# Kernel optimization log

Hardware: AMD Instinct MI355X
Metric: run time of the kernel (lower is better)

Reference implementation:

```python
import jax, jax.numpy as jnp
import numpy as np

EMBED_DIM = 400
HEAD_SIZE = 64


def setup_inputs() -> dict:
    key = jax.random.key(0)
    k1, k2, k3, k4 = jax.random.split(key, 4)
    B, T, C = 8, 2048, EMBED_DIM
    x = jax.random.normal(k1, (B, T, C), dtype=jnp.float32)
    # Linear(embed_dim, head_size, bias=False) weights, stored as [C, H] for x @ W
    s = 1.0 / np.sqrt(C)
    Wq = jax.random.uniform(k2, (C, HEAD_SIZE), dtype=jnp.float32, minval=-s, maxval=s)
    Wk = jax.random.uniform(k3, (C, HEAD_SIZE), dtype=jnp.float32, minval=-s, maxval=s)
    Wv = jax.random.uniform(k4, (C, HEAD_SIZE), dtype=jnp.float32, minval=-s, maxval=s)
    return {"x": x, "Wq": Wq, "Wk": Wk, "Wv": Wv}


def reference(x, Wq, Wk, Wv):
    B, T, C = x.shape
    q = x @ Wq  # [B,T,H]
    k = x @ Wk  # [B,T,H]
    v = x @ Wv  # [B,T,H]
    scale = 1.0 / jnp.sqrt(jnp.asarray(q.shape[-1], q.dtype))
    scores = jnp.einsum('bth,bsh->bts', q, k) * scale  # [B,T,T]
    causal = jnp.tril(jnp.ones((T, T), dtype=bool))
    scores = jnp.where(causal, scores, jnp.asarray(-jnp.inf, scores.dtype))
    attn = jax.nn.softmax(scores, axis=-1)
    out = jnp.einsum('bts,bsh->bth', attn, v)  # [B,T,H]
    return out
```

## Files before the change

kernel.cpp:

```cpp
#include <hip/hip_runtime.h>
#include <math.h>

#define B_SZ   8
#define T_SEQ  2048
#define C_DIM  400
#define H_DIM  64
#define NROWS  (B_SZ * T_SEQ)
#define QT_TILES (T_SEQ / 64)
#define KPAD   416
#define LDSTR  424
#define NCH    8
#define TPC    4

typedef short s8v  __attribute__((ext_vector_type(8)));
typedef float f32x4 __attribute__((ext_vector_type(4)));

__device__ __forceinline__ unsigned short f2bf(float f) {
    unsigned int u = __float_as_uint(f);
    u = (u + 0x7FFFu + ((u >> 16) & 1u)) >> 16;
    return (unsigned short)u;
}

__device__ __forceinline__ unsigned cvtpk_bf16(float lo, float hi) {
    unsigned r;
    asm("v_cvt_pk_bf16_f32 %0, %1, %2" : "=v"(r) : "v"(lo), "v"(hi));
    return r;
}

__global__ __launch_bounds__(256) void wprep_kernel(
    const float* __restrict__ Wq, const float* __restrict__ Wk,
    const float* __restrict__ Wv, unsigned short* __restrict__ Wt)
{
    int idx = blockIdx.x * 256 + threadIdx.x;
    if (idx >= 3 * H_DIM * KPAD) return;
    int m = idx / (H_DIM * KPAD);
    int r = idx - m * (H_DIM * KPAD);
    int h = r / KPAD;
    int k = r - h * KPAD;
    const float* W = (m == 0) ? Wq : (m == 1) ? Wk : Wv;
    float v = (k < C_DIM) ? W[k * H_DIM + h] : 0.0f;
    if (m == 0) v *= 0.125f * 1.44269504088896f;
    Wt[idx] = f2bf(v);
}

__global__ __launch_bounds__(256) void proj_kernel(
    const float* __restrict__ x, const unsigned short* __restrict__ Wt,
    unsigned short* __restrict__ Qb, unsigned short* __restrict__ Kb,
    unsigned short* __restrict__ Vt)
{
    __shared__ unsigned short xl[16 * LDSTR];
    const int tid = threadIdx.x;
    const int tile = blockIdx.x;

    const float4* __restrict__ x4 = (const float4*)x;
    for (int idx = tid; idx < 16 * 104; idx += 256) {
        int row = idx / 104, c4 = idx - row * 104;
        ushort4 w;
        if (c4 < 100) {
            float4 v = x4[(size_t)(tile * 16 + row) * 100 + c4];
            w.x = f2bf(v.x); w.y = f2bf(v.y); w.z = f2bf(v.z); w.w = f2bf(v.w);
        } else { w.x = w.y = w.z = w.w = 0; }
        *(ushort4*)&xl[row * LDSTR + c4 * 4] = w;
    }
    __syncthreads();

    const int w = tid >> 6, l = tid & 63;
    const int lr = l & 15, g = l >> 4;

    f32x4 acc[3];
    acc[0] = (f32x4)0.f; acc[1] = (f32x4)0.f; acc[2] = (f32x4)0.f;

    for (int ks = 0; ks < KPAD / 32; ++ks) {
        s8v a = *(const s8v*)&xl[lr * LDSTR + ks * 32 + g * 8];
#pragma unroll
        for (int fl = 0; fl < 3; ++fl) {
            int f = w * 3 + fl;
            int col = (f & 3) * 16 + lr;
            const s8v b = *(const s8v*)&Wt[((size_t)(f >> 2) * H_DIM + col) * KPAD
                                           + ks * 32 + g * 8];
            acc[fl] = __builtin_amdgcn_mfma_f32_16x16x32_bf16(a, b, acc[fl], 0, 0, 0);
        }
    }

#pragma unroll
    for (int fl = 0; fl < 3; ++fl) {
        int f = w * 3 + fl;
        int m = f >> 2, col = (f & 3) * 16 + lr;
#pragma unroll
        for (int r = 0; r < 4; ++r) {
            int row_g = tile * 16 + g * 4 + r;
            unsigned short bv = f2bf(acc[fl][r]);
            if (m == 0)      Qb[(size_t)row_g * H_DIM + col] = bv;
            else if (m == 1) Kb[(size_t)row_g * H_DIM + col] = bv;
            else {
                int b = row_g >> 11, t = row_g & 2047;
                Vt[((size_t)b * H_DIM + col) * T_SEQ + t] = bv;
            }
        }
    }
}

__global__ __launch_bounds__(256) void attn_kernel(
    const unsigned short* __restrict__ Qb, const unsigned short* __restrict__ Kb,
    const unsigned short* __restrict__ Vt,
    float* __restrict__ Opart, float* __restrict__ lpart)
{
    const int c  = blockIdx.x;
    const int qt = blockIdx.y;
    const int b  = blockIdx.z;
    if (c * TPC > qt) return;
    const int kt0 = c * TPC;
    const int kend = min(kt0 + (TPC - 1), qt);

    __shared__ char smem[2][16384];

    const int tid = threadIdx.x;
    const int w = tid >> 6, l = tid & 63;
    const int lr = l & 15, g = l >> 4;
    const int q0 = qt * 64 + w * 16;

    const int r0 = tid >> 3;
    const int ch = tid & 7;
    const int swz = (ch * 16) ^ ((r0 & 7) << 4);
    const char* const Kg = (const char*)(Kb + (size_t)b * T_SEQ * H_DIM);
    const char* const Vg = (const char*)(Vt + (size_t)b * H_DIM * T_SEQ);

    uint4 kA, kB, vA, vB;
    auto LD = [&](int kt) {
        kA = *(const uint4*)(Kg + (size_t)(kt * 64 + r0     ) * 128 + ch * 16);
        kB = *(const uint4*)(Kg + (size_t)(kt * 64 + r0 + 32) * 128 + ch * 16);
        vA = *(const uint4*)(Vg + (size_t)(r0     ) * 4096 + kt * 128 + ch * 16);
        vB = *(const uint4*)(Vg + (size_t)(r0 + 32) * 4096 + kt * 128 + ch * 16);
    };
    auto ST = [&](int buf) {
        char* Kl = smem[buf];
        char* Vl = smem[buf] + 8192;
        *(uint4*)(Kl + r0 * 128 + swz)        = kA;
        *(uint4*)(Kl + (r0 + 32) * 128 + swz) = kB;
        *(uint4*)(Vl + r0 * 128 + swz)        = vA;
        *(uint4*)(Vl + (r0 + 32) * 128 + swz) = vB;
    };

    s8v aq[2];
#pragma unroll
    for (int s = 0; s < 2; ++s)
        aq[s] = *(const s8v*)&Qb[((size_t)b * T_SEQ + q0 + lr) * H_DIM + s * 32 + g * 8];

    f32x4 acc[4];
#pragma unroll
    for (int f = 0; f < 4; ++f) acc[f] = (f32x4)0.f;
    float lsum = 0.f;

    LD(kt0); ST(0);
    __syncthreads();
    int cur = 0;

    for (int kt = kt0; kt <= kend; ++kt) {
        if (kt < kend) LD(kt + 1);
        char* const Kl = smem[cur];
        char* const Vl = smem[cur] + 8192;

        f32x4 sacc[4];
#pragma unroll
        for (int f = 0; f < 4; ++f) sacc[f] = (f32x4)0.f;
        __builtin_amdgcn_s_setprio(1);
#pragma unroll
        for (int f = 0; f < 4; ++f)
#pragma unroll
            for (int s = 0; s < 2; ++s) {
                const s8v ak = *(const s8v*)(Kl + (f * 16 + lr) * 128
                                             + (((s * 4 + g) * 16) ^ ((lr & 7) << 4)));
                sacc[f] = __builtin_amdgcn_mfma_f32_16x16x32_bf16(ak, aq[s], sacc[f], 0, 0, 0);
            }
        __builtin_amdgcn_s_setprio(0);

        float p[4][4];
        const bool diag = (kt == qt);
        const int q_my = q0 + lr;
#pragma unroll
        for (int f = 0; f < 4; ++f)
#pragma unroll
            for (int r = 0; r < 4; ++r) {
                float pv = __builtin_amdgcn_exp2f(sacc[f][r]);
                if (diag && (kt * 64 + f * 16 + g * 4 + r) > q_my) pv = 0.0f;
                p[f][r] = pv;
                lsum += pv;
            }

        s8v ap[2];
#pragma unroll
        for (int s = 0; s < 2; ++s) {
            unsigned Fa = cvtpk_bf16(p[2 * s][0],     p[2 * s][1]);
            unsigned Fb = cvtpk_bf16(p[2 * s][2],     p[2 * s][3]);
            unsigned Ga = cvtpk_bf16(p[2 * s + 1][0], p[2 * s + 1][1]);
            unsigned Gb = cvtpk_bf16(p[2 * s + 1][2], p[2 * s + 1][3]);
            asm("v_permlane32_swap_b32 %0, %1" : "+v"(Fa), "+v"(Ga));
            asm("v_permlane16_swap_b32 %0, %1" : "+v"(Fa), "+v"(Ga));
            asm("v_permlane32_swap_b32 %0, %1" : "+v"(Fb), "+v"(Gb));
            asm("v_permlane16_swap_b32 %0, %1" : "+v"(Fb), "+v"(Gb));
            unsigned wds[4] = { Fa, Fb, Ga, Gb };
            ap[s] = *(const s8v*)wds;
        }

        __builtin_amdgcn_s_setprio(1);
#pragma unroll
        for (int f = 0; f < 4; ++f)
#pragma unroll
            for (int s = 0; s < 2; ++s) {
                const s8v bv = *(const s8v*)(Vl + (f * 16 + lr) * 128
                                             + (((s * 4 + g) * 16) ^ ((lr & 7) << 4)));
                acc[f] = __builtin_amdgcn_mfma_f32_16x16x32_bf16(ap[s], bv, acc[f], 0, 0, 0);
            }
        __builtin_amdgcn_s_setprio(0);

        if (kt < kend) {
            ST(cur ^ 1);
            __syncthreads();
            cur ^= 1;
        }
    }

    lsum += __shfl_xor(lsum, 16, 64);
    lsum += __shfl_xor(lsum, 32, 64);

    const size_t pb = ((size_t)(b * QT_TILES + qt) * NCH + c);
#pragma unroll
    for (int f = 0; f < 4; ++f)
#pragma unroll
        for (int r = 0; r < 4; ++r)
            Opart[pb * 4096 + (w * 16 + g * 4 + r) * 64 + f * 16 + lr] = acc[f][r];
    if (l < 16)
        lpart[pb * 64 + w * 16 + l] = lsum;
}

__global__ __launch_bounds__(256) void combine_kernel(
    const float* __restrict__ Opart, const float* __restrict__ lpart,
    float* __restrict__ out)
{
    const int idx = blockIdx.x * 256 + threadIdx.x;
    const int row = idx >> 4, h4 = idx & 15;
    const int b = row >> 11, t = row & 2047;
    const int qt = t >> 6, r = t & 63;
    const int nch = (qt >> 2) + 1;

    const float4* __restrict__ Op4 = (const float4*)Opart;
    float4 os = make_float4(0.f, 0.f, 0.f, 0.f);
    float ls = 0.f;
    const size_t base = (size_t)(b * QT_TILES + qt) * NCH;
    for (int cc = 0; cc < nch; ++cc) {
        float4 v = Op4[(base + cc) * 1024 + r * 16 + h4];
        os.x += v.x; os.y += v.y; os.z += v.z; os.w += v.w;
        ls += lpart[(base + cc) * 64 + r];
    }
    float inv = 1.0f / ls;
    ((float4*)out)[idx] = make_float4(os.x * inv, os.y * inv, os.z * inv, os.w * inv);
}

extern "C" void kernel_launch(void* const* d_in, const int* in_sizes, int n_in,
                              void* d_out, int out_size, void* d_ws, size_t ws_size,
                              hipStream_t stream)
{
    const float* x  = (const float*)d_in[0];
    const float* Wq = (const float*)d_in[1];
    const float* Wk = (const float*)d_in[2];
    const float* Wv = (const float*)d_in[3];
    float* out = (float*)d_out;

    char* ws = (char*)d_ws;
    unsigned short* Wt = (unsigned short*)(ws);
    unsigned short* Qb = (unsigned short*)(ws + 163840);
    unsigned short* Kb = (unsigned short*)(ws + 163840 + 2097152);
    unsigned short* Vt = (unsigned short*)(ws + 163840 + 2 * 2097152);
    float* Opart = (float*)(ws + 163840 + 3 * 2097152);
    float* lpart = (float*)(ws + 163840 + 3 * 2097152 + 33554432);

    wprep_kernel<<<(3 * H_DIM * KPAD + 255) / 256, 256, 0, stream>>>(Wq, Wk, Wv, Wt);
    proj_kernel<<<NROWS / 16, 256, 0, stream>>>(x, Wt, Qb, Kb, Vt);
    attn_kernel<<<dim3(NCH, QT_TILES, B_SZ), 256, 0, stream>>>(Qb, Kb, Vt, Opart, lpart);
    combine_kernel<<<(NROWS * H_DIM / 4) / 256, 256, 0, stream>>>(Opart, lpart, out);
}
```

Baseline: 52.56 us.

## Enlarge query tile to 128 rows and projection tile to 64 rows

The attention kernel now handles 128 query rows per block, with each wave owning two 16-row fragments, so every K/V tile staged in LDS is reused across twice as many queries. The projection kernel processes 64 rows per block and reuses each weight fragment across four row groups. Together these cut global and LDS traffic per unit of work and halve the number of attention blocks. In exchange they raise register pressure, which can lower occupancy, and the larger causal tiles mean more masked wasted work on the diagonal.

Result: slower. 57.57 us (+9.5%).

```diff
diff --git a/kernel.cpp b/kernel.cpp
--- a/kernel.cpp
+++ b/kernel.cpp
@@ -6,7 +6,7 @@
 #define C_DIM  400
 #define H_DIM  64
 #define NROWS  (B_SZ * T_SEQ)
-#define QT_TILES (T_SEQ / 64)
+#define QT2    (T_SEQ / 128)
 #define KPAD   416
 #define LDSTR  424
 #define NCH    8
@@ -48,37 +48,45 @@
     unsigned short* __restrict__ Qb, unsigned short* __restrict__ Kb,
     unsigned short* __restrict__ Vt)
 {
-    __shared__ unsigned short xl[16 * LDSTR];
+    __shared__ unsigned short xl[64 * LDSTR];
     const int tid = threadIdx.x;
     const int tile = blockIdx.x;
 
     const float4* __restrict__ x4 = (const float4*)x;
-    for (int idx = tid; idx < 16 * 104; idx += 256) {
+    for (int idx = tid; idx < 64 * 104; idx += 256) {
         int row = idx / 104, c4 = idx - row * 104;
-        ushort4 w;
+        ushort4 wv;
         if (c4 < 100) {
-            float4 v = x4[(size_t)(tile * 16 + row) * 100 + c4];
-            w.x = f2bf(v.x); w.y = f2bf(v.y); w.z = f2bf(v.z); w.w = f2bf(v.w);
-        } else { w.x = w.y = w.z = w.w = 0; }
-        *(ushort4*)&xl[row * LDSTR + c4 * 4] = w;
+            float4 v = x4[(size_t)(tile * 64 + row) * 100 + c4];
+            wv.x = f2bf(v.x); wv.y = f2bf(v.y); wv.z = f2bf(v.z); wv.w = f2bf(v.w);
+        } else { wv.x = wv.y = wv.z = wv.w = 0; }
+        *(ushort4*)&xl[row * LDSTR + c4 * 4] = wv;
     }
     __syncthreads();
 
     const int w = tid >> 6, l = tid & 63;
     const int lr = l & 15, g = l >> 4;
 
-    f32x4 acc[3];
-    acc[0] = (f32x4)0.f; acc[1] = (f32x4)0.f; acc[2] = (f32x4)0.f;
+    f32x4 acc[3][4];
+#pragma unroll
+    for (int fl = 0; fl < 3; ++fl)
+#pragma unroll
+        for (int rg = 0; rg < 4; ++rg) acc[fl][rg] = (f32x4)0.f;
 
     for (int ks = 0; ks < KPAD / 32; ++ks) {
-        s8v a = *(const s8v*)&xl[lr * LDSTR + ks * 32 + g * 8];
+        s8v a[4];
+#pragma unroll
+        for (int rg = 0; rg < 4; ++rg)
+            a[rg] = *(const s8v*)&xl[(rg * 16 + lr) * LDSTR + ks * 32 + g * 8];
 #pragma unroll
         for (int fl = 0; fl < 3; ++fl) {
             int f = w * 3 + fl;
             int col = (f & 3) * 16 + lr;
             const s8v b = *(const s8v*)&Wt[((size_t)(f >> 2) * H_DIM + col) * KPAD
                                            + ks * 32 + g * 8];
-            acc[fl] = __builtin_amdgcn_mfma_f32_16x16x32_bf16(a, b, acc[fl], 0, 0, 0);
+#pragma unroll
+            for (int rg = 0; rg < 4; ++rg)
+                acc[fl][rg] = __builtin_amdgcn_mfma_f32_16x16x32_bf16(a[rg], b, acc[fl][rg], 0, 0, 0);
         }
     }
 
@@ -87,16 +95,18 @@
         int f = w * 3 + fl;
         int m = f >> 2, col = (f & 3) * 16 + lr;
 #pragma unroll
-        for (int r = 0; r < 4; ++r) {
-            int row_g = tile * 16 + g * 4 + r;
-            unsigned short bv = f2bf(acc[fl][r]);
-            if (m == 0)      Qb[(size_t)row_g * H_DIM + col] = bv;
-            else if (m == 1) Kb[(size_t)row_g * H_DIM + col] = bv;
-            else {
-                int b = row_g >> 11, t = row_g & 2047;
-                Vt[((size_t)b * H_DIM + col) * T_SEQ + t] = bv;
+        for (int rg = 0; rg < 4; ++rg)
+#pragma unroll
+            for (int r = 0; r < 4; ++r) {
+                int row_g = tile * 64 + rg * 16 + g * 4 + r;
+                unsigned short bv = f2bf(acc[fl][rg][r]);
+                if (m == 0)      Qb[(size_t)row_g * H_DIM + col] = bv;
+                else if (m == 1) Kb[(size_t)row_g * H_DIM + col] = bv;
+                else {
+                    int b = row_g >> 11, t = row_g & 2047;
+                    Vt[((size_t)b * H_DIM + col) * T_SEQ + t] = bv;
+                }
             }
-        }
     }
 }
 
@@ -105,19 +115,19 @@
     const unsigned short* __restrict__ Vt,
     float* __restrict__ Opart, float* __restrict__ lpart)
 {
-    const int c  = blockIdx.x;
-    const int qt = blockIdx.y;
-    const int b  = blockIdx.z;
-    if (c * TPC > qt) return;
+    const int c = blockIdx.x;
+    const int m = blockIdx.y;
+    const int b = blockIdx.z;
+    if (c * TPC > 2 * m + 1) return;
     const int kt0 = c * TPC;
-    const int kend = min(kt0 + (TPC - 1), qt);
+    const int kend = min(kt0 + (TPC - 1), 2 * m + 1);
 
     __shared__ char smem[2][16384];
 
     const int tid = threadIdx.x;
     const int w = tid >> 6, l = tid & 63;
     const int lr = l & 15, g = l >> 4;
-    const int q0 = qt * 64 + w * 16;
+    const int q0 = m * 128 + w * 32;
 
     const int r0 = tid >> 3;
     const int ch = tid & 7;
@@ -141,15 +151,20 @@
         *(uint4*)(Vl + (r0 + 32) * 128 + swz) = vB;
     };
 
-    s8v aq[2];
-#pragma unroll
-    for (int s = 0; s < 2; ++s)
-        aq[s] = *(const s8v*)&Qb[((size_t)b * T_SEQ + q0 + lr) * H_DIM + s * 32 + g * 8];
-
-    f32x4 acc[4];
-#pragma unroll
-    for (int f = 0; f < 4; ++f) acc[f] = (f32x4)0.f;
-    float lsum = 0.f;
+    s8v aq[2][2];
+#pragma unroll
+    for (int qf = 0; qf < 2; ++qf)
+#pragma unroll
+        for (int s = 0; s < 2; ++s)
+            aq[qf][s] = *(const s8v*)&Qb[((size_t)b * T_SEQ + q0 + qf * 16 + lr) * H_DIM
+                                         + s * 32 + g * 8];
+
+    f32x4 acc[2][4];
+#pragma unroll
+    for (int qf = 0; qf < 2; ++qf)
+#pragma unroll
+        for (int f = 0; f < 4; ++f) acc[qf][f] = (f32x4)0.f;
+    float lsum[2] = {0.f, 0.f};
 
     LD(kt0); ST(0);
     __syncthreads();
@@ -160,9 +175,11 @@
         char* const Kl = smem[cur];
         char* const Vl = smem[cur] + 8192;
 
-        f32x4 sacc[4];
-#pragma unroll
-        for (int f = 0; f < 4; ++f) sacc[f] = (f32x4)0.f;
+        f32x4 sacc[4][2];
+#pragma unroll
+        for (int f = 0; f < 4; ++f)
+#pragma unroll
+            for (int qf = 0; qf < 2; ++qf) sacc[f][qf] = (f32x4)0.f;
         __builtin_amdgcn_s_setprio(1);
 #pragma unroll
         for (int f = 0; f < 4; ++f)
@@ -170,37 +187,42 @@
             for (int s = 0; s < 2; ++s) {
                 const s8v ak = *(const s8v*)(Kl + (f * 16 + lr) * 128
                                              + (((s * 4 + g) * 16) ^ ((lr & 7) << 4)));
-                sacc[f] = __builtin_amdgcn_mfma_f32_16x16x32_bf16(ak, aq[s], sacc[f], 0, 0, 0);
+#pragma unroll
+                for (int qf = 0; qf < 2; ++qf)
+                    sacc[f][qf] = __builtin_amdgcn_mfma_f32_16x16x32_bf16(ak, aq[qf][s], sacc[f][qf], 0, 0, 0);
             }
         __builtin_amdgcn_s_setprio(0);
 
-        float p[4][4];
-        const bool diag = (kt == qt);
-        const int q_my = q0 + lr;
-#pragma unroll
-        for (int f = 0; f < 4; ++f)
-#pragma unroll
-            for (int r = 0; r < 4; ++r) {
-                float pv = __builtin_amdgcn_exp2f(sacc[f][r]);
-                if (diag && (kt * 64 + f * 16 + g * 4 + r) > q_my) pv = 0.0f;
-                p[f][r] = pv;
-                lsum += pv;
+        s8v ap[2][2];
+#pragma unroll
+        for (int s = 0; s < 2; ++s)
+#pragma unroll
+            for (int qf = 0; qf < 2; ++qf) {
+                const int q_my = q0 + qf * 16 + lr;
+                const bool dg = (kt * 64 + 63) > (q0 + qf * 16);
+                float p[8];
+#pragma unroll
+                for (int fh = 0; fh < 2; ++fh) {
+                    const int f = 2 * s + fh;
+#pragma unroll
+                    for (int r = 0; r < 4; ++r) {
+                        float pv = __builtin_amdgcn_exp2f(sacc[f][qf][r]);
+                        if (dg && (kt * 64 + f * 16 + g * 4 + r) > q_my) pv = 0.0f;
+                        p[fh * 4 + r] = pv;
+                        lsum[qf] += pv;
+                    }
+                }
+                unsigned Fa = cvtpk_bf16(p[0], p[1]);
+                unsigned Fb = cvtpk_bf16(p[2], p[3]);
+                unsigned Ga = cvtpk_bf16(p[4], p[5]);
+                unsigned Gb = cvtpk_bf16(p[6], p[7]);
+                asm("v_permlane32_swap_b32 %0, %1" : "+v"(Fa), "+v"(Ga));
+                asm("v_permlane16_swap_b32 %0, %1" : "+v"(Fa), "+v"(Ga));
+                asm("v_permlane32_swap_b32 %0, %1" : "+v"(Fb), "+v"(Gb));
+                asm("v_permlane16_swap_b32 %0, %1" : "+v"(Fb), "+v"(Gb));
+                unsigned wds[4] = { Fa, Fb, Ga, Gb };
+                ap[qf][s] = *(const s8v*)wds;
             }
-
-        s8v ap[2];
-#pragma unroll
-        for (int s = 0; s < 2; ++s) {
-            unsigned Fa = cvtpk_bf16(p[2 * s][0],     p[2 * s][1]);
-            unsigned Fb = cvtpk_bf16(p[2 * s][2],     p[2 * s][3]);
-            unsigned Ga = cvtpk_bf16(p[2 * s + 1][0], p[2 * s + 1][1]);
-            unsigned Gb = cvtpk_bf16(p[2 * s + 1][2], p[2 * s + 1][3]);
-            asm("v_permlane32_swap_b32 %0, %1" : "+v"(Fa), "+v"(Ga));
-            asm("v_permlane16_swap_b32 %0, %1" : "+v"(Fa), "+v"(Ga));
-            asm("v_permlane32_swap_b32 %0, %1" : "+v"(Fb), "+v"(Gb));
-            asm("v_permlane16_swap_b32 %0, %1" : "+v"(Fb), "+v"(Gb));
-            unsigned wds[4] = { Fa, Fb, Ga, Gb };
-            ap[s] = *(const s8v*)wds;
-        }
 
         __builtin_amdgcn_s_setprio(1);
 #pragma unroll
@@ -209,7 +231,9 @@
             for (int s = 0; s < 2; ++s) {
                 const s8v bv = *(const s8v*)(Vl + (f * 16 + lr) * 128
                                              + (((s * 4 + g) * 16) ^ ((lr & 7) << 4)));
-                acc[f] = __builtin_amdgcn_mfma_f32_16x16x32_bf16(ap[s], bv, acc[f], 0, 0, 0);
+#pragma unroll
+                for (int qf = 0; qf < 2; ++qf)
+                    acc[qf][f] = __builtin_amdgcn_mfma_f32_16x16x32_bf16(ap[qf][s], bv, acc[qf][f], 0, 0, 0);
             }
         __builtin_amdgcn_s_setprio(0);
 
@@ -220,17 +244,25 @@
         }
     }
 
-    lsum += __shfl_xor(lsum, 16, 64);
-    lsum += __shfl_xor(lsum, 32, 64);
-
-    const size_t pb = ((size_t)(b * QT_TILES + qt) * NCH + c);
-#pragma unroll
-    for (int f = 0; f < 4; ++f)
-#pragma unroll
-        for (int r = 0; r < 4; ++r)
-            Opart[pb * 4096 + (w * 16 + g * 4 + r) * 64 + f * 16 + lr] = acc[f][r];
-    if (l < 16)
-        lpart[pb * 64 + w * 16 + l] = lsum;
+#pragma unroll
+    for (int qf = 0; qf < 2; ++qf) {
+        lsum[qf] += __shfl_xor(lsum[qf], 16, 64);
+        lsum[qf] += __shfl_xor(lsum[qf], 32, 64);
+    }
+
+    const size_t pb = ((size_t)(b * QT2 + m) * NCH + c);
+#pragma unroll
+    for (int qf = 0; qf < 2; ++qf)
+#pragma unroll
+        for (int f = 0; f < 4; ++f)
+#pragma unroll
+            for (int r = 0; r < 4; ++r)
+                Opart[pb * 8192 + (w * 32 + qf * 16 + g * 4 + r) * 64 + f * 16 + lr]
+                    = acc[qf][f][r];
+    if (l < 16) {
+        lpart[pb * 128 + w * 32 + l]      = lsum[0];
+        lpart[pb * 128 + w * 32 + 16 + l] = lsum[1];
+    }
 }
 
 __global__ __launch_bounds__(256) void combine_kernel(
@@ -240,17 +272,17 @@
     const int idx = blockIdx.x * 256 + threadIdx.x;
     const int row = idx >> 4, h4 = idx & 15;
     const int b = row >> 11, t = row & 2047;
-    const int qt = t >> 6, r = t & 63;
-    const int nch = (qt >> 2) + 1;
+    const int m = t >> 7, r = t & 127;
+    const int nch = (m >> 1) + 1;
 
     const float4* __restrict__ Op4 = (const float4*)Opart;
     float4 os = make_float4(0.f, 0.f, 0.f, 0.f);
     float ls = 0.f;
-    const size_t base = (size_t)(b * QT_TILES + qt) * NCH;
+    const size_t base = (size_t)(b * QT2 + m) * NCH;
     for (int cc = 0; cc < nch; ++cc) {
-        float4 v = Op4[(base + cc) * 1024 + r * 16 + h4];
+        float4 v = Op4[(base + cc) * 2048 + r * 16 + h4];
         os.x += v.x; os.y += v.y; os.z += v.z; os.w += v.w;
-        ls += lpart[(base + cc) * 64 + r];
+        ls += lpart[(base + cc) * 128 + r];
     }
     float inv = 1.0f / ls;
     ((float4*)out)[idx] = make_float4(os.x * inv, os.y * inv, os.z * inv, os.w * inv);
@@ -275,7 +307,7 @@
     float* lpart = (float*)(ws + 163840 + 3 * 2097152 + 33554432);
 
     wprep_kernel<<<(3 * H_DIM * KPAD + 255) / 256, 256, 0, stream>>>(Wq, Wk, Wv, Wt);
-    proj_kernel<<<NROWS / 16, 256, 0, stream>>>(x, Wt, Qb, Kb, Vt);
-    attn_kernel<<<dim3(NCH, QT_TILES, B_SZ), 256, 0, stream>>>(Qb, Kb, Vt, Opart, lpart);
+    proj_kernel<<<NROWS / 64, 256, 0, stream>>>(x, Wt, Qb, Kb, Vt);
+    attn_kernel<<<dim3(NCH, QT2, B_SZ), 256, 0, stream>>>(Qb, Kb, Vt, Opart, lpart);
     combine_kernel<<<(NROWS * H_DIM / 4) / 256, 256, 0, stream>>>(Opart, lpart, out);
 }
```
